# Kernel tuning notes

Measured on AMD Instinct MI355X. Metric: run time of the kernel, lower is better.

## Reference

```python
import jax, jax.numpy as jnp
import numpy as np

B, T, D_MODEL, H = 4, 2048, 1024, 16
D_HEAD = D_MODEL // H
THETA = 10000.0


def setup_inputs() -> dict:
    key = jax.random.key(0)
    ks = jax.random.split(key, 5)
    s = 0.02
    return {
        "x": jax.random.normal(ks[0], (B, T, D_MODEL), dtype=jnp.float32),
        "Wq": jax.random.normal(ks[1], (D_MODEL, D_MODEL), dtype=jnp.float32) * s,
        "bq": jnp.zeros((D_MODEL,), dtype=jnp.float32),
        "Wk": jax.random.normal(ks[2], (D_MODEL, D_MODEL), dtype=jnp.float32) * s,
        "bk": jnp.zeros((D_MODEL,), dtype=jnp.float32),
        "Wv": jax.random.normal(ks[3], (D_MODEL, D_MODEL), dtype=jnp.float32) * s,
        "bv": jnp.zeros((D_MODEL,), dtype=jnp.float32),
        "Wo": jax.random.normal(ks[4], (D_MODEL, D_MODEL), dtype=jnp.float32) * s,
        "bo": jnp.zeros((D_MODEL,), dtype=jnp.float32),
    }


def _rope_tables(t_len, d_head, theta):
    inv_freq = 1.0 / theta ** (jnp.arange(0, d_head, 2, dtype=jnp.float32) / d_head)
    t = jnp.arange(t_len, dtype=jnp.float32)
    freqs = jnp.einsum('i,k->ik', t, inv_freq)  # [T, d_head/2]
    return jnp.cos(freqs), jnp.sin(freqs)


def _apply_rope(x, cos, sin):
    # x: [B, H, T, d_head]; cos/sin: [T, d_head/2] broadcast over B,H
    c = cos[None, None, :, :]
    s = sin[None, None, :, :]
    x0, x1 = x[..., ::2], x[..., 1::2]
    x_rot = jnp.stack((x0 * c - x1 * s, x0 * s + x1 * c), axis=-1)
    return x_rot.reshape(x.shape)


def reference(x, Wq, bq, Wk, bk, Wv, bv, Wo, bo):
    b, t, c = x.shape
    h, dh = H, D_HEAD
    q = (x @ Wq.T + bq).reshape(b, t, h, dh).transpose(0, 2, 1, 3)
    k = (x @ Wk.T + bk).reshape(b, t, h, dh).transpose(0, 2, 1, 3)
    v = (x @ Wv.T + bv).reshape(b, t, h, dh).transpose(0, 2, 1, 3)
    cos, sin = _rope_tables(t, dh, THETA)
    q = _apply_rope(q, cos, sin)
    k = _apply_rope(k, cos, sin)
    scores = jnp.einsum('bhqd,bhkd->bhqk', q, k) / jnp.sqrt(jnp.float32(dh))
    causal = jnp.tril(jnp.ones((t, t), dtype=bool))
    scores = jnp.where(causal[None, None, :, :], scores, -jnp.inf)
    attn = jax.nn.softmax(scores, axis=-1)
    out = jnp.einsum('bhqk,bhkd->bhqd', attn, v)
    out = out.transpose(0, 2, 1, 3).reshape(b, t, c)
    return out @ Wo.T + bo
```

## Files before the change

### kernel.cpp

```cpp
#include <hip/hip_runtime.h>
#include <hip/hip_bf16.h>

#define DEV static __device__ __forceinline__
#define AS1q __attribute__((address_space(1)))
#define AS3q __attribute__((address_space(3)))

typedef __attribute__((ext_vector_type(4))) float f32x4;
typedef __attribute__((ext_vector_type(16))) float f32x16;
typedef __attribute__((ext_vector_type(8))) short short8;
typedef __attribute__((ext_vector_type(4))) unsigned short u16x4;
typedef __attribute__((ext_vector_type(4))) unsigned int u32x4;

#define NB 4
#define NT 2048
#define NDM 1024
#define NH 16
#define NDH 64
#define NM (NB * NT)

DEV float bf2f(unsigned short u) {
  union { unsigned int i; float f; } x;
  x.i = ((unsigned int)u) << 16;
  return x.f;
}
DEV unsigned short f2bf(float f) {
  __hip_bfloat16 h = __float2bfloat16(f);
  return *reinterpret_cast<unsigned short*>(&h);
}
DEV unsigned int pack2bf(float lo, float hi) {
  return ((unsigned int)f2bf(hi) << 16) | (unsigned int)f2bf(lo);
}
DEV short8 mkfrag(unsigned int w0, unsigned int w1, unsigned int w2, unsigned int w3) {
  union { u32x4 u; short8 s; } x;
  x.u[0] = w0; x.u[1] = w1; x.u[2] = w2; x.u[3] = w3;
  return x.s;
}
DEV void permswap(unsigned int& a, unsigned int& b) {
  auto r = __builtin_amdgcn_permlane32_swap(a, b, false, false);
  a = r[0]; b = r[1];
}
DEV float dpp_swap1(float v) {
  union { float f; int i; } x; x.f = v;
  int r = __builtin_amdgcn_update_dpp(0, x.i, 0xB1, 0xF, 0xF, true);
  union { int i; float f; } y; y.i = r;
  return y.f;
}

__global__ __launch_bounds__(256) void k_cvt_bf16(const float* __restrict__ in,
                                                  unsigned short* __restrict__ out,
                                                  int n8) {
  int i = blockIdx.x * 256 + threadIdx.x;
  if (i >= n8) return;
  const f32x4* p = (const f32x4*)(in + (size_t)i * 8);
  f32x4 a = p[0], b = p[1];
  short8 o;
  o[0] = (short)f2bf(a[0]); o[1] = (short)f2bf(a[1]);
  o[2] = (short)f2bf(a[2]); o[3] = (short)f2bf(a[3]);
  o[4] = (short)f2bf(b[0]); o[5] = (short)f2bf(b[1]);
  o[6] = (short)f2bf(b[2]); o[7] = (short)f2bf(b[3]);
  *(short8*)(out + (size_t)i * 8) = o;
}

__global__ __launch_bounds__(256) void k_cvt_w(const float* __restrict__ w0, const float* __restrict__ w1,
                                               const float* __restrict__ w2, const float* __restrict__ w3,
                                               unsigned short* __restrict__ o0, unsigned short* __restrict__ o1,
                                               unsigned short* __restrict__ o2, unsigned short* __restrict__ o3) {
  int i = blockIdx.x * 256 + threadIdx.x;
  int m = blockIdx.y;
  const float* in = (m == 0) ? w0 : (m == 1) ? w1 : (m == 2) ? w2 : w3;
  unsigned short* out = (m == 0) ? o0 : (m == 1) ? o1 : (m == 2) ? o2 : o3;
  const f32x4* p = (const f32x4*)(in + (size_t)i * 8);
  f32x4 a = p[0], b = p[1];
  short8 o;
  o[0] = (short)f2bf(a[0]); o[1] = (short)f2bf(a[1]);
  o[2] = (short)f2bf(a[2]); o[3] = (short)f2bf(a[3]);
  o[4] = (short)f2bf(b[0]); o[5] = (short)f2bf(b[1]);
  o[6] = (short)f2bf(b[2]); o[7] = (short)f2bf(b[3]);
  *(short8*)(out + (size_t)i * 8) = o;
}

__global__ __launch_bounds__(256) void k_rope_table(float2* __restrict__ tab) {
  int i = blockIdx.x * 256 + threadIdx.x;
  int t = i >> 5, f = i & 31;
  float inv = powf(10000.0f, -(float)f / 32.0f);
  float ang = (float)t * inv;
  tab[i] = make_float2(cosf(ang), sinf(ang));
}

DEV void gemm_core(const unsigned short* __restrict__ Ab,
                   const unsigned short* __restrict__ Bb,
                   int Kdim, unsigned short* lds,
                   int tid, int wr, int wc, int lq, int gg,
                   f32x4 (&acc)[4][4]) {
  const int q0 = tid,       r0 = q0 >> 3; const int o0 = ((q0 & 7) ^ (r0 & 7)) * 8;
  const int q1 = tid + 256, r1 = q1 >> 3; const int o1 = ((q1 & 7) ^ (r1 & 7)) * 8;
  const int q2 = tid + 512, r2 = q2 >> 3; const int o2 = ((q2 & 7) ^ (r2 & 7)) * 8;
  const int q3 = tid + 768, r3 = q3 >> 3; const int o3 = ((q3 & 7) ^ (r3 & 7)) * 8;
  const unsigned short* pa0 = Ab + (size_t)r0 * Kdim + o0;
  const unsigned short* pa1 = Ab + (size_t)r1 * Kdim + o1;
  const unsigned short* pa2 = Ab + (size_t)r2 * Kdim + o2;
  const unsigned short* pa3 = Ab + (size_t)r3 * Kdim + o3;
  const unsigned short* pb0 = Bb + (size_t)r0 * Kdim + o0;
  const unsigned short* pb1 = Bb + (size_t)r1 * Kdim + o1;
  const unsigned short* pb2 = Bb + (size_t)r2 * Kdim + o2;
  const unsigned short* pb3 = Bb + (size_t)r3 * Kdim + o3;
  const int e0 = q0 * 8, e1 = q1 * 8, e2 = q2 * 8, e3 = q3 * 8;

  auto stage = [&](int buf, int ko) {
    unsigned short* LA = lds + buf * 8192;
    unsigned short* LB = lds + 16384 + buf * 8192;
    __builtin_amdgcn_global_load_lds((const AS1q void*)(pa0 + ko), (AS3q void*)(LA + e0), 16, 0, 0);
    __builtin_amdgcn_global_load_lds((const AS1q void*)(pa1 + ko), (AS3q void*)(LA + e1), 16, 0, 0);
    __builtin_amdgcn_global_load_lds((const AS1q void*)(pa2 + ko), (AS3q void*)(LA + e2), 16, 0, 0);
    __builtin_amdgcn_global_load_lds((const AS1q void*)(pa3 + ko), (AS3q void*)(LA + e3), 16, 0, 0);
    __builtin_amdgcn_global_load_lds((const AS1q void*)(pb0 + ko), (AS3q void*)(LB + e0), 16, 0, 0);
    __builtin_amdgcn_global_load_lds((const AS1q void*)(pb1 + ko), (AS3q void*)(LB + e1), 16, 0, 0);
    __builtin_amdgcn_global_load_lds((const AS1q void*)(pb2 + ko), (AS3q void*)(LB + e2), 16, 0, 0);
    __builtin_amdgcn_global_load_lds((const AS1q void*)(pb3 + ko), (AS3q void*)(LB + e3), 16, 0, 0);
  };

  const int xA = (wr + lq) & 7, xB = (wc + lq) & 7;
  const int rowA = (wr + lq) * 64, rowB = (wc + lq) * 64;
  const int cA0 = (gg ^ xA) * 8, cA1 = ((4 + gg) ^ xA) * 8;
  const int cB0 = (gg ^ xB) * 8, cB1 = ((4 + gg) ^ xB) * 8;

  const int NKT = Kdim >> 6;
  stage(0, 0);
  __syncthreads();
  int cur = 0;
  for (int t = 0; t < NKT; ++t) {
    if (t + 1 < NKT) stage(cur ^ 1, (t + 1) << 6);
    const unsigned short* LA = lds + cur * 8192;
    const unsigned short* LB = lds + 16384 + cur * 8192;
    short8 af[4], bf[4];
#pragma unroll
    for (int i = 0; i < 4; ++i) af[i] = *(const short8*)&LA[rowA + i * 1024 + cA0];
#pragma unroll
    for (int j = 0; j < 4; ++j) bf[j] = *(const short8*)&LB[rowB + j * 1024 + cB0];
#pragma unroll
    for (int i = 0; i < 4; ++i)
#pragma unroll
      for (int j = 0; j < 4; ++j)
        acc[i][j] = __builtin_amdgcn_mfma_f32_16x16x32_bf16(af[i], bf[j], acc[i][j], 0, 0, 0);
#pragma unroll
    for (int i = 0; i < 4; ++i) af[i] = *(const short8*)&LA[rowA + i * 1024 + cA1];
#pragma unroll
    for (int j = 0; j < 4; ++j) bf[j] = *(const short8*)&LB[rowB + j * 1024 + cB1];
#pragma unroll
    for (int i = 0; i < 4; ++i)
#pragma unroll
      for (int j = 0; j < 4; ++j)
        acc[i][j] = __builtin_amdgcn_mfma_f32_16x16x32_bf16(af[i], bf[j], acc[i][j], 0, 0, 0);
    __syncthreads();
    cur ^= 1;
  }
}

__global__ __launch_bounds__(256) void k_gemm_qkv(const unsigned short* __restrict__ A,
                                                  const unsigned short* __restrict__ Bw,
                                                  const float* __restrict__ bq,
                                                  const float* __restrict__ bk,
                                                  const float* __restrict__ bv,
                                                  const float2* __restrict__ tab,
                                                  unsigned short* __restrict__ QH,
                                                  unsigned short* __restrict__ KH,
                                                  unsigned short* __restrict__ VT) {
  __shared__ unsigned short lds[4 * 8192];
  const int K = NDM;
  const int tid = threadIdx.x;
  const int lane = tid & 63;
  const int wave = tid >> 6;
  const int wr = (wave >> 1) * 64;
  const int wc = (wave & 1) * 64;
  const int lq = lane & 15;
  const int gg = lane >> 4;

  unsigned int nbx = gridDim.x;
  unsigned int bid = blockIdx.y * nbx + blockIdx.x;
  unsigned int cpx = (nbx * gridDim.y) >> 3;
  unsigned int swz = (bid & 7) * cpx + (bid >> 3);
  const int bn = swz % nbx, bm = swz / nbx;

  const unsigned short* Ab = A + (size_t)bm * 128 * K;
  const unsigned short* Bb = Bw + (size_t)bn * 128 * K;

  f32x4 acc[4][4] = {};
  gemm_core(Ab, Bb, K, lds, tid, wr, wc, lq, gg, acc);

  const int which = bn >> 3;
  const int nloc = (bn & 7) * 128;
  const int rowb = bm * 128 + wr + (lane >> 4) * 4;
  const int colb = nloc + wc + lq;

  if (which == 2) {
#pragma unroll
    for (int i = 0; i < 4; ++i) {
#pragma unroll
      for (int j = 0; j < 4; ++j) {
        const int col = colb + j * 16;
        const float bs = bv[col];
        const int h = col >> 6, dh = col & 63;
        u16x4 w;
#pragma unroll
        for (int r = 0; r < 4; ++r) w[r] = f2bf(acc[i][j][r] + bs);
        const int row = rowb + i * 16;
        const int bb = row >> 11, t = row & (NT - 1);
        *(u16x4*)&VT[(((size_t)(bb * NH + h)) * NDH + dh) * NT + t] = w;
      }
    }
  } else {
    const float* bias = which ? bk : bq;
    unsigned short* Out = which ? KH : QH;
    const float sc = which ? 1.0f : 0.125f * 1.44269504088896f;
#pragma unroll
    for (int i = 0; i < 4; ++i) {
#pragma unroll
      for (int j = 0; j < 4; ++j) {
        const int col = colb + j * 16;
        const float bs = bias[col];
        const int h = col >> 6, dh = col & 63;
        const int pidx = dh >> 1;
        const bool odd = dh & 1;
#pragma unroll
        for (int r = 0; r < 4; ++r) {
          const int row = rowb + i * 16 + r;
          const int bb = row >> 11, t = row & (NT - 1);
          const float v = acc[i][j][r] + bs;
          const float pv = dpp_swap1(v);
          const float2 cs = tab[t * 32 + pidx];
          const float y = odd ? (pv * cs.y + v * cs.x) : (v * cs.x - pv * cs.y);
          Out[(((size_t)(bb * NH + h)) * NT + t) * NDH + dh] = f2bf(y * sc);
        }
      }
    }
  }
}

__global__ __launch_bounds__(256) void k_gemm_bt(const unsigned short* __restrict__ A,
                                                 const unsigned short* __restrict__ Bw,
                                                 const float* __restrict__ bias,
                                                 float* __restrict__ Cout,
                                                 int M, int N, int K) {
  __shared__ unsigned short lds[4 * 8192];
  const int tid = threadIdx.x;
  const int lane = tid & 63;
  const int wave = tid >> 6;
  const int wr = (wave >> 1) * 64;
  const int wc = (wave & 1) * 64;
  const int lq = lane & 15;
  const int gg = lane >> 4;

  unsigned int nbx = gridDim.x;
  unsigned int bid = blockIdx.y * nbx + blockIdx.x;
  unsigned int cpx = (nbx * gridDim.y) >> 3;
  unsigned int swz = (bid & 7) * cpx + (bid >> 3);
  const int bn = swz % nbx, bm = swz / nbx;

  const unsigned short* Ab = A + (size_t)bm * 128 * K;
  const unsigned short* Bb = Bw + (size_t)bn * 128 * K;

  f32x4 acc[4][4] = {};
  gemm_core(Ab, Bb, K, lds, tid, wr, wc, lq, gg, acc);

  const int rowb = bm * 128 + wr + (lane >> 4) * 4;
  const int colb = bn * 128 + wc + lq;
#pragma unroll
  for (int i = 0; i < 4; ++i) {
#pragma unroll
    for (int j = 0; j < 4; ++j) {
      const int col = colb + j * 16;
      const float bs = bias[col];
#pragma unroll
      for (int r = 0; r < 4; ++r) {
        const size_t idx = (size_t)(rowb + i * 16 + r) * N + col;
        Cout[idx] = acc[i][j][r] + bs;
      }
    }
  }
}

__global__ __launch_bounds__(256, 2) void k_attn(const unsigned short* __restrict__ Qh,
                                                 const unsigned short* __restrict__ Kh,
                                                 const unsigned short* __restrict__ Vtp,
                                                 unsigned short* __restrict__ Ctx) {
  __shared__ unsigned short kl[2][64 * 64];
  __shared__ unsigned short vl[2][64 * 64];
  const int tid = threadIdx.x;
  const int wave = tid >> 6, lane = tid & 63;
  const int l31 = lane & 31, hi = lane >> 5;
  const int b0 = blockIdx.x;
  const int bh = (b0 & 7) * 8 + ((b0 >> 3) & 7);
  const int t = 15 - (b0 >> 6);
  const int b = bh >> 4, h = bh & 15;

  const unsigned short* K = Kh + (size_t)bh * NT * NDH;
  const unsigned short* V = Vtp + (size_t)bh * NDH * NT;

  const int ch0 = tid, ch1 = tid + 256;
  const int sr0 = ch0 >> 3, sc0 = ((ch0 & 7) ^ (sr0 & 7)) * 8;
  const int sr1 = ch1 >> 3, sc1 = ((ch1 & 7) ^ (sr1 & 7)) * 8;
  const int xe = (l31 & 7) << 3;

  auto stage = [&](int buf, int kv0) {
    __builtin_amdgcn_global_load_lds(
        (const AS1q void*)(K + (size_t)(kv0 + sr0) * NDH + sc0),
        (AS3q void*)(&kl[buf][ch0 * 8]), 16, 0, 0);
    __builtin_amdgcn_global_load_lds(
        (const AS1q void*)(K + (size_t)(kv0 + sr1) * NDH + sc1),
        (AS3q void*)(&kl[buf][ch1 * 8]), 16, 0, 0);
    __builtin_amdgcn_global_load_lds(
        (const AS1q void*)(V + (size_t)sr0 * NT + kv0 + sc0),
        (AS3q void*)(&vl[buf][ch0 * 8]), 16, 0, 0);
    __builtin_amdgcn_global_load_lds(
        (const AS1q void*)(V + (size_t)sr1 * NT + kv0 + sc1),
        (AS3q void*)(&vl[buf][ch1 * 8]), 16, 0, 0);
  };

  const int q0w = t * 128 + wave * 32;
  const int nkv = 2 * t + 2;

  const unsigned short* Qr = Qh + ((size_t)bh * NT + q0w + l31) * NDH + 8 * hi;
  short8 qf[4];
#pragma unroll
  for (int s = 0; s < 4; ++s) qf[s] = *(const short8*)&Qr[16 * s];

  short8 onesf;
#pragma unroll
  for (int s = 0; s < 8; ++s) onesf[s] = (short)0x3F80;

  f32x16 ot0 = {}, ot1 = {}, lacc = {};

  stage(0, 0);
  __syncthreads();

  for (int kb = 0; kb < nkv; ++kb) {
    const int cur = kb & 1;
    const int kv0 = kb * 64;
    if (kb + 1 < nkv) stage(cur ^ 1, kv0 + 64);

    if (kv0 <= q0w + 31) {
      const unsigned short* kc = kl[cur];
      f32x16 st0 = {}, st1 = {};
#pragma unroll
      for (int s = 0; s < 4; ++s) {
        const int co = (16 * s + 8 * hi) ^ xe;
        short8 k0 = *(const short8*)&kc[l31 * 64 + co];
        short8 k1 = *(const short8*)&kc[(32 + l31) * 64 + co];
        st0 = __builtin_amdgcn_mfma_f32_32x32x16_bf16(k0, qf[s], st0, 0, 0, 0);
        st1 = __builtin_amdgcn_mfma_f32_32x32x16_bf16(k1, qf[s], st1, 0, 0, 0);
      }
      if (kv0 + 64 > q0w) {
        const int qg = q0w + l31;
#pragma unroll
        for (int r = 0; r < 16; ++r) {
          const int kr = kv0 + (r & 3) + 8 * (r >> 2) + 4 * hi;
          if (kr > qg) st0[r] = -1e30f;
          if (kr + 32 > qg) st1[r] = -1e30f;
        }
      }
#pragma unroll
      for (int r = 0; r < 16; ++r) st0[r] = exp2f(st0[r]);
#pragma unroll
      for (int r = 0; r < 16; ++r) st1[r] = exp2f(st1[r]);
      short8 pf[4];
#pragma unroll
      for (int ks = 0; ks < 4; ++ks) {
        const f32x16& sm = (ks & 2) ? st1 : st0;
        const int o = (ks & 1) * 8;
        unsigned int w0 = pack2bf(sm[o + 0], sm[o + 1]);
        unsigned int w2 = pack2bf(sm[o + 4], sm[o + 5]);
        permswap(w0, w2);
        unsigned int w1 = pack2bf(sm[o + 2], sm[o + 3]);
        unsigned int w3 = pack2bf(sm[o + 6], sm[o + 7]);
        permswap(w1, w3);
        pf[ks] = mkfrag(w0, w1, w2, w3);
      }
      const unsigned short* vc = vl[cur];
#pragma unroll
      for (int ks = 0; ks < 4; ++ks) {
        const int co = (16 * ks + 8 * hi) ^ xe;
        short8 v0 = *(const short8*)&vc[l31 * 64 + co];
        short8 v1 = *(const short8*)&vc[(32 + l31) * 64 + co];
        ot0 = __builtin_amdgcn_mfma_f32_32x32x16_bf16(v0, pf[ks], ot0, 0, 0, 0);
        ot1 = __builtin_amdgcn_mfma_f32_32x32x16_bf16(v1, pf[ks], ot1, 0, 0, 0);
        lacc = __builtin_amdgcn_mfma_f32_32x32x16_bf16(onesf, pf[ks], lacc, 0, 0, 0);
      }
    }
    __syncthreads();
  }

  const float inv_l = 1.0f / lacc[0];
  unsigned short* dst = Ctx + ((size_t)(b * NT) + q0w + l31) * NDM + h * NDH;
#pragma unroll
  for (int dt = 0; dt < 2; ++dt) {
#pragma unroll
    for (int grp = 0; grp < 4; ++grp) {
      u16x4 w;
#pragma unroll
      for (int r = 0; r < 4; ++r) {
        const float v = (dt ? ot1[grp * 4 + r] : ot0[grp * 4 + r]) * inv_l;
        w[r] = f2bf(v);
      }
      *(u16x4*)&dst[dt * 32 + grp * 8 + 4 * hi] = w;
    }
  }
}

extern "C" void kernel_launch(void* const* d_in, const int* in_sizes, int n_in,
                              void* d_out, int out_size, void* d_ws, size_t ws_size,
                              hipStream_t stream) {
  const float* x  = (const float*)d_in[0];
  const float* Wq = (const float*)d_in[1];
  const float* bq = (const float*)d_in[2];
  const float* Wk = (const float*)d_in[3];
  const float* bk = (const float*)d_in[4];
  const float* Wv = (const float*)d_in[5];
  const float* bv = (const float*)d_in[6];
  const float* Wo = (const float*)d_in[7];
  const float* bo = (const float*)d_in[8];

  char* ws = (char*)d_ws;
  const size_t MB = 1024 * 1024;
  if (ws_size < 90 * MB) return;

  unsigned short* XB   = (unsigned short*)(ws + 0);
  unsigned short* WQB  = (unsigned short*)(ws + 16 * MB);
  unsigned short* WKB  = (unsigned short*)(ws + 18 * MB);
  unsigned short* WVB  = (unsigned short*)(ws + 20 * MB);
  unsigned short* WOB  = (unsigned short*)(ws + 22 * MB);
  unsigned short* QH   = (unsigned short*)(ws + 24 * MB);
  unsigned short* KH   = (unsigned short*)(ws + 40 * MB);
  unsigned short* VT   = (unsigned short*)(ws + 56 * MB);
  unsigned short* CTX  = (unsigned short*)(ws + 72 * MB);
  float2* TAB          = (float2*)(ws + 88 * MB);

  k_cvt_bf16<<<(NM * NDM / 8) / 256, 256, 0, stream>>>(x, XB, NM * NDM / 8);
  dim3 gw((NDM * NDM / 8) / 256, 4);
  k_cvt_w<<<gw, 256, 0, stream>>>(Wq, Wk, Wv, Wo, WQB, WKB, WVB, WOB);
  k_rope_table<<<(NT * 32) / 256, 256, 0, stream>>>(TAB);

  dim3 gq(3 * NDM / 128, NM / 128);
  k_gemm_qkv<<<gq, 256, 0, stream>>>(XB, WQB, bq, bk, bv, TAB, QH, KH, VT);

  k_attn<<<NB * NH * 16, 256, 0, stream>>>(QH, KH, VT, CTX);

  dim3 go(NDM / 128, NM / 128);
  k_gemm_bt<<<go, 256, 0, stream>>>(CTX, WOB, bo, (float*)d_out, NM, NDM, NDM);
}
```

Measured before the change: 181.3 us.

## Halve GEMM K-tile to 32 and add MFMA priority hints in attention

```diff
diff --git a/kernel.cpp b/kernel.cpp
--- a/kernel.cpp
+++ b/kernel.cpp
@@ -92,60 +92,39 @@
                    int Kdim, unsigned short* lds,
                    int tid, int wr, int wc, int lq, int gg,
                    f32x4 (&acc)[4][4]) {
-  const int q0 = tid,       r0 = q0 >> 3; const int o0 = ((q0 & 7) ^ (r0 & 7)) * 8;
-  const int q1 = tid + 256, r1 = q1 >> 3; const int o1 = ((q1 & 7) ^ (r1 & 7)) * 8;
-  const int q2 = tid + 512, r2 = q2 >> 3; const int o2 = ((q2 & 7) ^ (r2 & 7)) * 8;
-  const int q3 = tid + 768, r3 = q3 >> 3; const int o3 = ((q3 & 7) ^ (r3 & 7)) * 8;
+  const int c0 = tid,       r0 = c0 >> 2; const int o0 = ((c0 & 3) ^ (r0 & 3)) * 8;
+  const int c1 = tid + 256, r1 = c1 >> 2; const int o1 = ((c1 & 3) ^ (r1 & 3)) * 8;
   const unsigned short* pa0 = Ab + (size_t)r0 * Kdim + o0;
   const unsigned short* pa1 = Ab + (size_t)r1 * Kdim + o1;
-  const unsigned short* pa2 = Ab + (size_t)r2 * Kdim + o2;
-  const unsigned short* pa3 = Ab + (size_t)r3 * Kdim + o3;
   const unsigned short* pb0 = Bb + (size_t)r0 * Kdim + o0;
   const unsigned short* pb1 = Bb + (size_t)r1 * Kdim + o1;
-  const unsigned short* pb2 = Bb + (size_t)r2 * Kdim + o2;
-  const unsigned short* pb3 = Bb + (size_t)r3 * Kdim + o3;
-  const int e0 = q0 * 8, e1 = q1 * 8, e2 = q2 * 8, e3 = q3 * 8;
+  const int e0 = c0 * 8, e1 = c1 * 8;
 
   auto stage = [&](int buf, int ko) {
-    unsigned short* LA = lds + buf * 8192;
-    unsigned short* LB = lds + 16384 + buf * 8192;
+    unsigned short* LA = lds + buf * 4096;
+    unsigned short* LB = lds + 8192 + buf * 4096;
     __builtin_amdgcn_global_load_lds((const AS1q void*)(pa0 + ko), (AS3q void*)(LA + e0), 16, 0, 0);
     __builtin_amdgcn_global_load_lds((const AS1q void*)(pa1 + ko), (AS3q void*)(LA + e1), 16, 0, 0);
-    __builtin_amdgcn_global_load_lds((const AS1q void*)(pa2 + ko), (AS3q void*)(LA + e2), 16, 0, 0);
-    __builtin_amdgcn_global_load_lds((const AS1q void*)(pa3 + ko), (AS3q void*)(LA + e3), 16, 0, 0);
     __builtin_amdgcn_global_load_lds((const AS1q void*)(pb0 + ko), (AS3q void*)(LB + e0), 16, 0, 0);
     __builtin_amdgcn_global_load_lds((const AS1q void*)(pb1 + ko), (AS3q void*)(LB + e1), 16, 0, 0);
-    __builtin_amdgcn_global_load_lds((const AS1q void*)(pb2 + ko), (AS3q void*)(LB + e2), 16, 0, 0);
-    __builtin_amdgcn_global_load_lds((const AS1q void*)(pb3 + ko), (AS3q void*)(LB + e3), 16, 0, 0);
   };
 
-  const int xA = (wr + lq) & 7, xB = (wc + lq) & 7;
-  const int rowA = (wr + lq) * 64, rowB = (wc + lq) * 64;
-  const int cA0 = (gg ^ xA) * 8, cA1 = ((4 + gg) ^ xA) * 8;
-  const int cB0 = (gg ^ xB) * 8, cB1 = ((4 + gg) ^ xB) * 8;
-
-  const int NKT = Kdim >> 6;
+  const int rowA = (wr + lq) * 32, rowB = (wc + lq) * 32;
+  const int cAB = ((gg ^ (lq & 3)) & 3) * 8;
+
+  const int NKT = Kdim >> 5;
   stage(0, 0);
   __syncthreads();
   int cur = 0;
   for (int t = 0; t < NKT; ++t) {
-    if (t + 1 < NKT) stage(cur ^ 1, (t + 1) << 6);
-    const unsigned short* LA = lds + cur * 8192;
-    const unsigned short* LB = lds + 16384 + cur * 8192;
+    if (t + 1 < NKT) stage(cur ^ 1, (t + 1) << 5);
+    const unsigned short* LA = lds + cur * 4096;
+    const unsigned short* LB = lds + 8192 + cur * 4096;
     short8 af[4], bf[4];
 #pragma unroll
-    for (int i = 0; i < 4; ++i) af[i] = *(const short8*)&LA[rowA + i * 1024 + cA0];
-#pragma unroll
-    for (int j = 0; j < 4; ++j) bf[j] = *(const short8*)&LB[rowB + j * 1024 + cB0];
-#pragma unroll
-    for (int i = 0; i < 4; ++i)
-#pragma unroll
-      for (int j = 0; j < 4; ++j)
-        acc[i][j] = __builtin_amdgcn_mfma_f32_16x16x32_bf16(af[i], bf[j], acc[i][j], 0, 0, 0);
-#pragma unroll
-    for (int i = 0; i < 4; ++i) af[i] = *(const short8*)&LA[rowA + i * 1024 + cA1];
-#pragma unroll
-    for (int j = 0; j < 4; ++j) bf[j] = *(const short8*)&LB[rowB + j * 1024 + cB1];
+    for (int i = 0; i < 4; ++i) af[i] = *(const short8*)&LA[rowA + i * 512 + cAB];
+#pragma unroll
+    for (int j = 0; j < 4; ++j) bf[j] = *(const short8*)&LB[rowB + j * 512 + cAB];
 #pragma unroll
     for (int i = 0; i < 4; ++i)
 #pragma unroll
@@ -165,7 +144,7 @@
                                                   unsigned short* __restrict__ QH,
                                                   unsigned short* __restrict__ KH,
                                                   unsigned short* __restrict__ VT) {
-  __shared__ unsigned short lds[4 * 8192];
+  __shared__ unsigned short lds[4 * 4096];
   const int K = NDM;
   const int tid = threadIdx.x;
   const int lane = tid & 63;
@@ -241,7 +220,7 @@
                                                  const float* __restrict__ bias,
                                                  float* __restrict__ Cout,
                                                  int M, int N, int K) {
-  __shared__ unsigned short lds[4 * 8192];
+  __shared__ unsigned short lds[4 * 4096];
   const int tid = threadIdx.x;
   const int lane = tid & 63;
   const int wave = tid >> 6;
@@ -341,6 +320,7 @@
     if (kv0 <= q0w + 31) {
       const unsigned short* kc = kl[cur];
       f32x16 st0 = {}, st1 = {};
+      __builtin_amdgcn_s_setprio(1);
 #pragma unroll
       for (int s = 0; s < 4; ++s) {
         const int co = (16 * s + 8 * hi) ^ xe;
@@ -349,6 +329,7 @@
         st0 = __builtin_amdgcn_mfma_f32_32x32x16_bf16(k0, qf[s], st0, 0, 0, 0);
         st1 = __builtin_amdgcn_mfma_f32_32x32x16_bf16(k1, qf[s], st1, 0, 0, 0);
       }
+      __builtin_amdgcn_s_setprio(0);
       if (kv0 + 64 > q0w) {
         const int qg = q0w + l31;
 #pragma unroll
@@ -376,6 +357,7 @@
         pf[ks] = mkfrag(w0, w1, w2, w3);
       }
       const unsigned short* vc = vl[cur];
+      __builtin_amdgcn_s_setprio(1);
 #pragma unroll
       for (int ks = 0; ks < 4; ++ks) {
         const int co = (16 * ks + 8 * hi) ^ xe;
@@ -385,6 +367,7 @@
         ot1 = __builtin_amdgcn_mfma_f32_32x32x16_bf16(v1, pf[ks], ot1, 0, 0, 0);
         lacc = __builtin_amdgcn_mfma_f32_32x32x16_bf16(onesf, pf[ks], lacc, 0, 0, 0);
       }
+      __builtin_amdgcn_s_setprio(0);
     }
     __syncthreads();
   }
```

Result: slower. 194.1 us (+7.1%).
